# Optimization experiments

Hardware: AMD Instinct MI355X
Metric: run time of the kernel (lower is better)

Reference implementation:

```python
import jax, jax.numpy as jnp
import numpy as np

P = 64       # number of pathways
NV = 512     # features per pathway (nvar[i])
W = 256      # hidden width per pathway
COV = 16     # covariates
B = 2048     # batch
EPS = 1e-5   # BatchNorm eps
SLOPE = 0.2  # LeakyReLU negative slope


def _lrelu(v):
    return jnp.where(v >= 0, v, SLOPE * v)


def setup_inputs() -> dict:
    key = jax.random.key(0)
    ks = jax.random.split(key, 8)
    x = jax.random.normal(ks[0], (B, P * NV + COV), dtype=jnp.float32)
    # per-pathway weights (no bias), stacked across pathways -> grouped GEMM
    W1 = jax.random.normal(ks[1], (P, NV, W), dtype=jnp.float32) * (1.0 / np.sqrt(NV))
    W2 = jax.random.normal(ks[2], (P, W, W), dtype=jnp.float32) * (1.0 / np.sqrt(W))
    W3 = jax.random.normal(ks[3], (P, W), dtype=jnp.float32) * (1.0 / np.sqrt(W))
    gamma = jnp.ones((P,), dtype=jnp.float32)   # bn_path weight
    beta = jnp.zeros((P,), dtype=jnp.float32)   # bn_path bias
    fc_w = jax.random.normal(ks[4], (P + COV, 1), dtype=jnp.float32) * 0.05
    fc_b = jnp.full((1,), 0.001, dtype=jnp.float32)
    return {"x": x, "W1": W1, "W2": W2, "W3": W3,
            "gamma": gamma, "beta": beta, "fc_w": fc_w, "fc_b": fc_b}


def reference(x, W1, W2, W3, gamma, beta, fc_w, fc_b):
    # pathway blocks (dropout = identity in eval): grouped GEMMs over P pathways
    xp = x[:, : P * NV].reshape(B, P, NV)
    h = _lrelu(jnp.einsum('bpi,pio->bpo', xp, W1))
    h = _lrelu(jnp.einsum('bpi,pio->bpo', h, W2))
    p = _lrelu(jnp.einsum('bpi,pi->bp', h, W3))          # [B, P]
    # BatchNorm1d (training-mode batch statistics, biased variance)
    mean = p.mean(axis=0)
    var = p.var(axis=0)
    pn = (p - mean) / jnp.sqrt(var + EPS) * gamma + beta
    # global L2 (Frobenius) normalization, as torch.norm(pathway_layer, 2)
    pn = pn / jnp.linalg.norm(pn)
    # concat covariates, final linear + sigmoid
    z = jnp.concatenate([pn, x[:, P * NV: P * NV + COV]], axis=1)  # [B, P+COV]
    return jax.nn.sigmoid(z @ fc_w + fc_b)                         # [B, 1]
```

## Files before the change

### kernel.cpp

```cpp
#include <hip/hip_runtime.h>
#include <hip/hip_bf16.h>

#define PW 64
#define NV 512
#define HW 256
#define COV 16
#define BATCH 2048
#define XROW (PW * NV + COV)
#define IMG 16384

typedef short s16x8 __attribute__((ext_vector_type(8)));
typedef float f32x4 __attribute__((ext_vector_type(4)));

__device__ __forceinline__ unsigned short f2bf(float f) {
    union { float f; unsigned int u; } v;
    v.f = f;
    unsigned int u = v.u;
    unsigned int r = (u + 0x7fffu + ((u >> 16) & 1u)) >> 16;
    return (unsigned short)r;
}

__device__ __forceinline__ unsigned int pack2(float a, float b) {
    __hip_bfloat162 h = __float22bfloat162_rn(float2{a, b});
    union { __hip_bfloat162 h; unsigned int u; } c;
    c.h = h;
    return c.u;
}

__device__ __forceinline__ float lrelu(float v) { return v >= 0.f ? v : 0.2f * v; }

__device__ __forceinline__ void gl_lds16(const void* g, void* l) {
    __builtin_amdgcn_global_load_lds(
        (const __attribute__((address_space(1))) void*)g,
        (__attribute__((address_space(3))) void*)l, 16, 0, 0);
}

__global__ __launch_bounds__(256)
void transpose_all(const float* __restrict__ W1, const float* __restrict__ W2,
                   unsigned short* __restrict__ W1I, unsigned short* __restrict__ W2I) {
    __shared__ float tile[64][260];
    int bx = blockIdx.x;
    const float* src;
    unsigned short* dst;
    if (bx < 512) {
        int p = bx >> 3, kb = bx & 7;
        src = W1 + ((size_t)p * NV + kb * 64) * HW;
        dst = W1I + (size_t)(p * 8 + kb) * IMG;
    } else {
        bx -= 512;
        int p = bx >> 2, kb = bx & 3;
        src = W2 + ((size_t)p * HW + kb * 64) * HW;
        dst = W2I + (size_t)(p * 4 + kb) * IMG;
    }
    const int t = threadIdx.x;
    #pragma unroll
    for (int i = 0; i < 16; ++i) {
        int idx = t + i * 256;
        int r = idx >> 6, c4 = (idx & 63) << 2;
        *(float4*)&tile[r][c4] = *(const float4*)(src + (size_t)r * HW + c4);
    }
    __syncthreads();
    #pragma unroll
    for (int pass = 0; pass < 8; ++pass) {
        int idx = pass * 256 + t;
        int n = idx >> 3, s = idx & 7;
        int g = s ^ (n & 7);
        unsigned short v[8];
        #pragma unroll
        for (int j = 0; j < 8; ++j)
            v[j] = f2bf(tile[g * 8 + j][n]);
        *(s16x8*)(dst + (size_t)idx * 8) = *(s16x8*)v;
    }
}

__global__ __launch_bounds__(256, 2)
void pathway_fused(const float* __restrict__ x, const unsigned short* __restrict__ W1I,
                   const unsigned short* __restrict__ W2I, const float* __restrict__ W3,
                   float* __restrict__ pvec) {
    __shared__ __align__(16) unsigned short As[64][72];
    __shared__ __align__(16) unsigned short Bs[256 * 64];
    __shared__ __align__(16) unsigned short H1t[64][264];
    __shared__ float red[4][64];

    const int lin = blockIdx.x + blockIdx.y * (BATCH / 64);
    const int xcd = lin & 7;
    const int idx0 = lin >> 3;
    const int p   = xcd * 8 + (idx0 >> 5);
    const int bm0 = (idx0 & 31) * 64;

    const int t = threadIdx.x;
    const int lane = t & 63;
    const int wave = t >> 6;
    const int wn   = wave * 64;
    const int l15  = lane & 15;
    const int quad = lane >> 4;

    const float* Ap          = x   + (size_t)p * NV;
    const unsigned short* B1 = W1I + (size_t)p * 8 * IMG;
    const unsigned short* B2 = W2I + (size_t)p * 4 * IMG;

    {
        float4 aReg[4];
        #pragma unroll
        for (int i = 0; i < 4; ++i) {
            int ii = t + i * 256, row = ii >> 4, c4 = (ii & 15) * 4;
            aReg[i] = *(const float4*)(Ap + (size_t)(bm0 + row) * XROW + c4);
        }
        f32x4 acc[4][4] = {};
        for (int k0 = 0; k0 < NV; k0 += 64) {
            #pragma unroll
            for (int i = 0; i < 4; ++i) {
                int ii = t + i * 256, row = ii >> 4, c4 = (ii & 15) * 4;
                uint2 u;
                u.x = pack2(aReg[i].x, aReg[i].y);
                u.y = pack2(aReg[i].z, aReg[i].w);
                *(uint2*)&As[row][c4] = u;
            }
            {
                const unsigned short* img = B1 + (size_t)(k0 >> 6) * IMG;
                #pragma unroll
                for (int c = 0; c < 8; ++c) {
                    int off = wave * 8192 + c * 1024;
                    gl_lds16((const char*)img + off + lane * 16, (char*)Bs + off);
                }
            }
            __syncthreads();
            if (k0 + 64 < NV) {
                #pragma unroll
                for (int i = 0; i < 4; ++i) {
                    int ii = t + i * 256, row = ii >> 4, c4 = (ii & 15) * 4;
                    aReg[i] = *(const float4*)(Ap + (size_t)(bm0 + row) * XROW + k0 + 64 + c4);
                }
            }
            #pragma unroll
            for (int kk = 0; kk < 64; kk += 32) {
                s16x8 af[4], bfr[4];
                #pragma unroll
                for (int mi = 0; mi < 4; ++mi)
                    af[mi] = *(const s16x8*)&As[mi * 16 + l15][kk + quad * 8];
                #pragma unroll
                for (int ni = 0; ni < 4; ++ni) {
                    int row  = wn + ni * 16 + l15;
                    int slot = ((kk >> 3) + quad) ^ (row & 7);
                    bfr[ni] = *(const s16x8*)&Bs[row * 64 + slot * 8];
                }
                #pragma unroll
                for (int mi = 0; mi < 4; ++mi)
                    #pragma unroll
                    for (int ni = 0; ni < 4; ++ni)
                        acc[mi][ni] = __builtin_amdgcn_mfma_f32_16x16x32_bf16(
                            af[mi], bfr[ni], acc[mi][ni], 0, 0, 0);
            }
            __syncthreads();
        }
        #pragma unroll
        for (int mi = 0; mi < 4; ++mi)
            #pragma unroll
            for (int ni = 0; ni < 4; ++ni)
                #pragma unroll
                for (int r = 0; r < 4; ++r)
                    H1t[mi * 16 + quad * 4 + r][wn + ni * 16 + l15] =
                        f2bf(lrelu(acc[mi][ni][r]));
    }
    __syncthreads();

    f32x4 acc2[4][4] = {};
    for (int k0 = 0; k0 < HW; k0 += 64) {
        const unsigned short* img = B2 + (size_t)(k0 >> 6) * IMG;
        #pragma unroll
        for (int c = 0; c < 8; ++c) {
            int off = wave * 8192 + c * 1024;
            gl_lds16((const char*)img + off + lane * 16, (char*)Bs + off);
        }
        __syncthreads();
        #pragma unroll
        for (int kk = 0; kk < 64; kk += 32) {
            s16x8 af[4], bfr[4];
            #pragma unroll
            for (int mi = 0; mi < 4; ++mi)
                af[mi] = *(const s16x8*)&H1t[mi * 16 + l15][k0 + kk + quad * 8];
            #pragma unroll
            for (int ni = 0; ni < 4; ++ni) {
                int row  = wn + ni * 16 + l15;
                int slot = ((kk >> 3) + quad) ^ (row & 7);
                bfr[ni] = *(const s16x8*)&Bs[row * 64 + slot * 8];
            }
            #pragma unroll
            for (int mi = 0; mi < 4; ++mi)
                #pragma unroll
                for (int ni = 0; ni < 4; ++ni)
                    acc2[mi][ni] = __builtin_amdgcn_mfma_f32_16x16x32_bf16(
                        af[mi], bfr[ni], acc2[mi][ni], 0, 0, 0);
        }
        __syncthreads();
    }

    float w3v[4];
    #pragma unroll
    for (int ni = 0; ni < 4; ++ni)
        w3v[ni] = W3[(size_t)p * HW + wn + ni * 16 + l15];
    float part[4][4];
    #pragma unroll
    for (int mi = 0; mi < 4; ++mi) {
        #pragma unroll
        for (int r = 0; r < 4; ++r) {
            float s = 0.f;
            #pragma unroll
            for (int ni = 0; ni < 4; ++ni)
                s += lrelu(acc2[mi][ni][r]) * w3v[ni];
            part[mi][r] = s;
        }
    }
    #pragma unroll
    for (int off = 1; off < 16; off <<= 1)
        #pragma unroll
        for (int mi = 0; mi < 4; ++mi)
            #pragma unroll
            for (int r = 0; r < 4; ++r)
                part[mi][r] += __shfl_xor(part[mi][r], off);
    if (l15 == 0)
        #pragma unroll
        for (int mi = 0; mi < 4; ++mi)
            #pragma unroll
            for (int r = 0; r < 4; ++r)
                red[wave][mi * 16 + quad * 4 + r] = part[mi][r];
    __syncthreads();
    if (t < 64) {
        float s = red[0][t] + red[1][t] + red[2][t] + red[3][t];
        pvec[(size_t)p * BATCH + bm0 + t] = lrelu(s);
    }
}

__global__ __launch_bounds__(256)
void stats_k(const float* __restrict__ pvec, float* __restrict__ stat) {
    const int p = blockIdx.x;
    float s = 0.f, q = 0.f;
    for (int i = threadIdx.x; i < BATCH; i += 256) {
        float v = pvec[(size_t)p * BATCH + i];
        s += v; q += v * v;
    }
    #pragma unroll
    for (int off = 32; off; off >>= 1) {
        s += __shfl_down(s, off);
        q += __shfl_down(q, off);
    }
    __shared__ float ls[4], lq[4];
    const int wave = threadIdx.x >> 6, lane = threadIdx.x & 63;
    if (lane == 0) { ls[wave] = s; lq[wave] = q; }
    __syncthreads();
    if (threadIdx.x == 0) {
        float S = ls[0] + ls[1] + ls[2] + ls[3];
        float Q = lq[0] + lq[1] + lq[2] + lq[3];
        float mean = S * (1.f / BATCH);
        float var  = Q * (1.f / BATCH) - mean * mean;
        stat[p]       = mean;
        stat[64 + p]  = rsqrtf(var + 1e-5f);
        stat[128 + p] = var;
    }
}

__global__ __launch_bounds__(256)
void final_k(const float* __restrict__ pvec, const float* __restrict__ stat,
             const float* __restrict__ gamma, const float* __restrict__ beta,
             const float* __restrict__ x, const float* __restrict__ fc_w,
             const float* __restrict__ fc_b, float* __restrict__ out) {
    const int b = blockIdx.x * 256 + threadIdx.x;
    float nsq = 0.f;
    #pragma unroll
    for (int p = 0; p < PW; ++p) {
        float g = gamma[p], bt = beta[p], var = stat[128 + p], inv = stat[64 + p];
        nsq += (float)BATCH * (g * g * var * inv * inv + bt * bt);
    }
    const float rn = rsqrtf(nsq);
    float acc = fc_b[0];
    #pragma unroll
    for (int p = 0; p < PW; ++p) {
        float pn = (pvec[(size_t)p * BATCH + b] - stat[p]) * stat[64 + p] * gamma[p] + beta[p];
        acc += pn * rn * fc_w[p];
    }
    #pragma unroll
    for (int c = 0; c < COV; ++c)
        acc += x[(size_t)b * XROW + PW * NV + c] * fc_w[PW + c];
    out[b] = 1.f / (1.f + __expf(-acc));
}

extern "C" void kernel_launch(void* const* d_in, const int* in_sizes, int n_in,
                              void* d_out, int out_size, void* d_ws, size_t ws_size,
                              hipStream_t stream) {
    const float* x     = (const float*)d_in[0];
    const float* W1    = (const float*)d_in[1];
    const float* W2    = (const float*)d_in[2];
    const float* W3    = (const float*)d_in[3];
    const float* gamma = (const float*)d_in[4];
    const float* beta  = (const float*)d_in[5];
    const float* fc_w  = (const float*)d_in[6];
    const float* fc_b  = (const float*)d_in[7];
    float* out = (float*)d_out;

    char* ws = (char*)d_ws;
    size_t off = 0;
    unsigned short* W1I = (unsigned short*)(ws + off); off += (size_t)PW * NV * HW * 2;
    unsigned short* W2I = (unsigned short*)(ws + off); off += (size_t)PW * HW * HW * 2;
    float* pvec = (float*)(ws + off); off += (size_t)PW * BATCH * 4;
    float* stat = (float*)(ws + off); off += 256 * 4;

    transpose_all<<<dim3(512 + 256), 256, 0, stream>>>(W1, W2, W1I, W2I);

    pathway_fused<<<dim3(BATCH / 64, PW), 256, 0, stream>>>(x, W1I, W2I, W3, pvec);

    stats_k<<<PW, 256, 0, stream>>>(pvec, stat);

    final_k<<<BATCH / 256, 256, 0, stream>>>(pvec, stat, gamma, beta, x, fc_w, fc_b, out);
}
```

Baseline: 480.2 us.

## Split fused pathway kernel into double-buffered GEMM1 and GEMM2 kernels via bf16 intermediate

Splits the fused two-layer pathway kernel into two kernels. The first layer's bf16 activations now go to a global workspace in swizzled 64x64 tiles that the second kernel loads straight to LDS. Both kernels double-buffer their A and B tiles in shared memory, so the next k-slice's global loads overlap the current MFMA work instead of stalling on a single buffer. The cost is a 64 MB global round trip for the hidden activations and an extra kernel launch.

```diff
diff --git a/kernel.cpp b/kernel.cpp
--- a/kernel.cpp
+++ b/kernel.cpp
@@ -8,6 +8,7 @@
 #define BATCH 2048
 #define XROW (PW * NV + COV)
 #define IMG 16384
+#define AIMG 4096
 
 typedef short s16x8 __attribute__((ext_vector_type(8)));
 typedef float f32x4 __attribute__((ext_vector_type(4)));
@@ -74,19 +75,17 @@
 }
 
 __global__ __launch_bounds__(256, 2)
-void pathway_fused(const float* __restrict__ x, const unsigned short* __restrict__ W1I,
-                   const unsigned short* __restrict__ W2I, const float* __restrict__ W3,
-                   float* __restrict__ pvec) {
-    __shared__ __align__(16) unsigned short As[64][72];
-    __shared__ __align__(16) unsigned short Bs[256 * 64];
-    __shared__ __align__(16) unsigned short H1t[64][264];
-    __shared__ float red[4][64];
-
-    const int lin = blockIdx.x + blockIdx.y * (BATCH / 64);
+void gemm1(const float* __restrict__ x, const unsigned short* __restrict__ W1I,
+           unsigned short* __restrict__ H1I) {
+    __shared__ __align__(16) unsigned short As[2][64 * 64];
+    __shared__ __align__(16) unsigned short Bs[2][256 * 64];
+
+    const int lin = blockIdx.x;
     const int xcd = lin & 7;
-    const int idx0 = lin >> 3;
-    const int p   = xcd * 8 + (idx0 >> 5);
-    const int bm0 = (idx0 & 31) * 64;
+    const int idx = lin >> 3;
+    const int p   = xcd * 8 + (idx >> 5);
+    const int m   = idx & 31;
+    const int bm0 = m * 64;
 
     const int t = threadIdx.x;
     const int lane = t & 63;
@@ -97,104 +96,176 @@
 
     const float* Ap          = x   + (size_t)p * NV;
     const unsigned short* B1 = W1I + (size_t)p * 8 * IMG;
-    const unsigned short* B2 = W2I + (size_t)p * 4 * IMG;
-
-    {
-        float4 aReg[4];
-        #pragma unroll
-        for (int i = 0; i < 4; ++i) {
-            int ii = t + i * 256, row = ii >> 4, c4 = (ii & 15) * 4;
-            aReg[i] = *(const float4*)(Ap + (size_t)(bm0 + row) * XROW + c4);
-        }
-        f32x4 acc[4][4] = {};
-        for (int k0 = 0; k0 < NV; k0 += 64) {
+
+    int arow[4], acol[4], aoff[4];
+    #pragma unroll
+    for (int i = 0; i < 4; ++i) {
+        int ii = t + i * 256;
+        arow[i] = ii >> 4;
+        acol[i] = (ii & 15) * 4;
+        int slot = (acol[i] >> 3) ^ (arow[i] & 7);
+        aoff[i] = arow[i] * 64 + slot * 8 + (acol[i] & 7);
+    }
+
+    float4 aA[4], aB[4];
+
+#define XLOAD(dst, k0) { \
+    _Pragma("unroll") \
+    for (int i = 0; i < 4; ++i) \
+        dst[i] = *(const float4*)(Ap + (size_t)(bm0 + arow[i]) * XROW + (k0) + acol[i]); }
+
+#define APACK(src, buf) { \
+    _Pragma("unroll") \
+    for (int i = 0; i < 4; ++i) { \
+        uint2 u; \
+        u.x = pack2(src[i].x, src[i].y); \
+        u.y = pack2(src[i].z, src[i].w); \
+        *(uint2*)&As[buf][aoff[i]] = u; } }
+
+#define B1STAGE(buf, kb) { \
+    const unsigned short* img = B1 + (size_t)(kb) * IMG; \
+    _Pragma("unroll") \
+    for (int c = 0; c < 8; ++c) { \
+        int off = wave * 8192 + c * 1024; \
+        gl_lds16((const char*)img + off + lane * 16, (char*)Bs[buf] + off); } }
+
+#define MFMA1(buf) { \
+    _Pragma("unroll") \
+    for (int kk = 0; kk < 64; kk += 32) { \
+        s16x8 af[4], bfr[4]; \
+        _Pragma("unroll") \
+        for (int mi = 0; mi < 4; ++mi) { \
+            int row = mi * 16 + l15; \
+            int slot = ((kk >> 3) + quad) ^ (row & 7); \
+            af[mi] = *(const s16x8*)&As[buf][row * 64 + slot * 8]; } \
+        _Pragma("unroll") \
+        for (int ni = 0; ni < 4; ++ni) { \
+            int row = wn + ni * 16 + l15; \
+            int slot = ((kk >> 3) + quad) ^ (row & 7); \
+            bfr[ni] = *(const s16x8*)&Bs[buf][row * 64 + slot * 8]; } \
+        _Pragma("unroll") \
+        for (int mi = 0; mi < 4; ++mi) \
+            _Pragma("unroll") \
+            for (int ni = 0; ni < 4; ++ni) \
+                acc[mi][ni] = __builtin_amdgcn_mfma_f32_16x16x32_bf16( \
+                    af[mi], bfr[ni], acc[mi][ni], 0, 0, 0); } }
+
+    XLOAD(aA, 0);
+    B1STAGE(0, 0);
+    APACK(aA, 0);
+    XLOAD(aA, 64);
+    __syncthreads();
+
+    f32x4 acc[4][4] = {};
+
+    #pragma unroll
+    for (int s2 = 0; s2 < 4; ++s2) {
+        const int te = 2 * s2;
+        if (te + 1 < 8) B1STAGE((te + 1) & 1, te + 1);
+        if (te + 2 < 8) XLOAD(aB, (te + 2) * 64);
+        MFMA1(te & 1);
+        if (te + 1 < 8) APACK(aA, (te + 1) & 1);
+        __syncthreads();
+        const int to = te + 1;
+        if (to + 1 < 8) B1STAGE((to + 1) & 1, to + 1);
+        if (to + 2 < 8) XLOAD(aA, (to + 2) * 64);
+        MFMA1(to & 1);
+        if (to + 1 < 8) APACK(aB, (to + 1) & 1);
+        __syncthreads();
+    }
+
+    unsigned short* Hp = H1I + ((size_t)(p * 32 + m) * 4 + wave) * AIMG;
+    #pragma unroll
+    for (int mi = 0; mi < 4; ++mi)
+        #pragma unroll
+        for (int ni = 0; ni < 4; ++ni)
             #pragma unroll
-            for (int i = 0; i < 4; ++i) {
-                int ii = t + i * 256, row = ii >> 4, c4 = (ii & 15) * 4;
-                uint2 u;
-                u.x = pack2(aReg[i].x, aReg[i].y);
-                u.y = pack2(aReg[i].z, aReg[i].w);
-                *(uint2*)&As[row][c4] = u;
+            for (int r = 0; r < 4; ++r) {
+                int row = mi * 16 + quad * 4 + r;
+                int col = ni * 16 + l15;
+                int slot = (col >> 3) ^ (row & 7);
+                Hp[row * 64 + slot * 8 + (col & 7)] = f2bf(lrelu(acc[mi][ni][r]));
             }
-            {
-                const unsigned short* img = B1 + (size_t)(k0 >> 6) * IMG;
-                #pragma unroll
-                for (int c = 0; c < 8; ++c) {
-                    int off = wave * 8192 + c * 1024;
-                    gl_lds16((const char*)img + off + lane * 16, (char*)Bs + off);
-                }
-            }
-            __syncthreads();
-            if (k0 + 64 < NV) {
-                #pragma unroll
-                for (int i = 0; i < 4; ++i) {
-                    int ii = t + i * 256, row = ii >> 4, c4 = (ii & 15) * 4;
-                    aReg[i] = *(const float4*)(Ap + (size_t)(bm0 + row) * XROW + k0 + 64 + c4);
-                }
-            }
-            #pragma unroll
-            for (int kk = 0; kk < 64; kk += 32) {
-                s16x8 af[4], bfr[4];
-                #pragma unroll
-                for (int mi = 0; mi < 4; ++mi)
-                    af[mi] = *(const s16x8*)&As[mi * 16 + l15][kk + quad * 8];
-                #pragma unroll
-                for (int ni = 0; ni < 4; ++ni) {
-                    int row  = wn + ni * 16 + l15;
-                    int slot = ((kk >> 3) + quad) ^ (row & 7);
-                    bfr[ni] = *(const s16x8*)&Bs[row * 64 + slot * 8];
-                }
-                #pragma unroll
-                for (int mi = 0; mi < 4; ++mi)
-                    #pragma unroll
-                    for (int ni = 0; ni < 4; ++ni)
-                        acc[mi][ni] = __builtin_amdgcn_mfma_f32_16x16x32_bf16(
-                            af[mi], bfr[ni], acc[mi][ni], 0, 0, 0);
-            }
-            __syncthreads();
-        }
-        #pragma unroll
-        for (int mi = 0; mi < 4; ++mi)
-            #pragma unroll
-            for (int ni = 0; ni < 4; ++ni)
-                #pragma unroll
-                for (int r = 0; r < 4; ++r)
-                    H1t[mi * 16 + quad * 4 + r][wn + ni * 16 + l15] =
-                        f2bf(lrelu(acc[mi][ni][r]));
-    }
-    __syncthreads();
-
-    f32x4 acc2[4][4] = {};
-    for (int k0 = 0; k0 < HW; k0 += 64) {
-        const unsigned short* img = B2 + (size_t)(k0 >> 6) * IMG;
-        #pragma unroll
-        for (int c = 0; c < 8; ++c) {
-            int off = wave * 8192 + c * 1024;
-            gl_lds16((const char*)img + off + lane * 16, (char*)Bs + off);
-        }
+#undef XLOAD
+#undef APACK
+#undef B1STAGE
+#undef MFMA1
+}
+
+__global__ __launch_bounds__(256, 2)
+void gemm2(const unsigned short* __restrict__ H1I, const unsigned short* __restrict__ W2I,
+           const float* __restrict__ W3, float* __restrict__ pvec) {
+    __shared__ __align__(16) unsigned short As[2][64 * 64];
+    __shared__ __align__(16) unsigned short Bs[2][256 * 64];
+
+    const int lin = blockIdx.x;
+    const int xcd = lin & 7;
+    const int idx = lin >> 3;
+    const int p   = xcd * 8 + (idx >> 5);
+    const int m   = idx & 31;
+    const int bm0 = m * 64;
+
+    const int t = threadIdx.x;
+    const int lane = t & 63;
+    const int wave = t >> 6;
+    const int wn   = wave * 64;
+    const int l15  = lane & 15;
+    const int quad = lane >> 4;
+
+    const unsigned short* Aimg = H1I + (size_t)(p * 32 + m) * 4 * AIMG;
+    const unsigned short* B2   = W2I + (size_t)p * 4 * IMG;
+
+#define A2STAGE(buf, kb) { \
+    const unsigned short* img = Aimg + (size_t)(kb) * AIMG; \
+    _Pragma("unroll") \
+    for (int c = 0; c < 2; ++c) { \
+        int off = wave * 2048 + c * 1024; \
+        gl_lds16((const char*)img + off + lane * 16, (char*)As[buf] + off); } }
+
+#define B2STAGE(buf, kb) { \
+    const unsigned short* img = B2 + (size_t)(kb) * IMG; \
+    _Pragma("unroll") \
+    for (int c = 0; c < 8; ++c) { \
+        int off = wave * 8192 + c * 1024; \
+        gl_lds16((const char*)img + off + lane * 16, (char*)Bs[buf] + off); } }
+
+#define MFMA2(buf) { \
+    _Pragma("unroll") \
+    for (int kk = 0; kk < 64; kk += 32) { \
+        s16x8 af[4], bfr[4]; \
+        _Pragma("unroll") \
+        for (int mi = 0; mi < 4; ++mi) { \
+            int row = mi * 16 + l15; \
+            int slot = ((kk >> 3) + quad) ^ (row & 7); \
+            af[mi] = *(const s16x8*)&As[buf][row * 64 + slot * 8]; } \
+        _Pragma("unroll") \
+        for (int ni = 0; ni < 4; ++ni) { \
+            int row = wn + ni * 16 + l15; \
+            int slot = ((kk >> 3) + quad) ^ (row & 7); \
+            bfr[ni] = *(const s16x8*)&Bs[buf][row * 64 + slot * 8]; } \
+        _Pragma("unroll") \
+        for (int mi = 0; mi < 4; ++mi) \
+            _Pragma("unroll") \
+            for (int ni = 0; ni < 4; ++ni) \
+                acc[mi][ni] = __builtin_amdgcn_mfma_f32_16x16x32_bf16( \
+                    af[mi], bfr[ni], acc[mi][ni], 0, 0, 0); } }
+
+    A2STAGE(0, 0);
+    B2STAGE(0, 0);
+    __syncthreads();
+
+    f32x4 acc[4][4] = {};
+    #pragma unroll
+    for (int t4 = 0; t4 < 4; ++t4) {
+        if (t4 + 1 < 4) { A2STAGE((t4 + 1) & 1, t4 + 1); B2STAGE((t4 + 1) & 1, t4 + 1); }
+        MFMA2(t4 & 1);
         __syncthreads();
-        #pragma unroll
-        for (int kk = 0; kk < 64; kk += 32) {
-            s16x8 af[4], bfr[4];
-            #pragma unroll
-            for (int mi = 0; mi < 4; ++mi)
-                af[mi] = *(const s16x8*)&H1t[mi * 16 + l15][k0 + kk + quad * 8];
-            #pragma unroll
-            for (int ni = 0; ni < 4; ++ni) {
-                int row  = wn + ni * 16 + l15;
-                int slot = ((kk >> 3) + quad) ^ (row & 7);
-                bfr[ni] = *(const s16x8*)&Bs[row * 64 + slot * 8];
-            }
-            #pragma unroll
-            for (int mi = 0; mi < 4; ++mi)
-                #pragma unroll
-                for (int ni = 0; ni < 4; ++ni)
-                    acc2[mi][ni] = __builtin_amdgcn_mfma_f32_16x16x32_bf16(
-                        af[mi], bfr[ni], acc2[mi][ni], 0, 0, 0);
-        }
-        __syncthreads();
-    }
-
+    }
+#undef A2STAGE
+#undef B2STAGE
+#undef MFMA2
+
+    float* red = (float*)&As[0][0];
     float w3v[4];
     #pragma unroll
     for (int ni = 0; ni < 4; ++ni)
@@ -207,7 +278,7 @@
             float s = 0.f;
             #pragma unroll
             for (int ni = 0; ni < 4; ++ni)
-                s += lrelu(acc2[mi][ni][r]) * w3v[ni];
+                s += lrelu(acc[mi][ni][r]) * w3v[ni];
             part[mi][r] = s;
         }
     }
@@ -223,10 +294,10 @@
         for (int mi = 0; mi < 4; ++mi)
             #pragma unroll
             for (int r = 0; r < 4; ++r)
-                red[wave][mi * 16 + quad * 4 + r] = part[mi][r];
+                red[wave * 64 + mi * 16 + quad * 4 + r] = part[mi][r];
     __syncthreads();
     if (t < 64) {
-        float s = red[0][t] + red[1][t] + red[2][t] + red[3][t];
+        float s = red[0 * 64 + t] + red[1 * 64 + t] + red[2 * 64 + t] + red[3 * 64 + t];
         pvec[(size_t)p * BATCH + bm0 + t] = lrelu(s);
     }
 }
@@ -301,12 +372,15 @@
     size_t off = 0;
     unsigned short* W1I = (unsigned short*)(ws + off); off += (size_t)PW * NV * HW * 2;
     unsigned short* W2I = (unsigned short*)(ws + off); off += (size_t)PW * HW * HW * 2;
+    unsigned short* H1I = (unsigned short*)(ws + off); off += (size_t)PW * BATCH * HW * 2;
     float* pvec = (float*)(ws + off); off += (size_t)PW * BATCH * 4;
     float* stat = (float*)(ws + off); off += 256 * 4;
 
     transpose_all<<<dim3(512 + 256), 256, 0, stream>>>(W1, W2, W1I, W2I);
 
-    pathway_fused<<<dim3(BATCH / 64, PW), 256, 0, stream>>>(x, W1I, W2I, W3, pvec);
+    gemm1<<<dim3(2048), 256, 0, stream>>>(x, W1I, H1I);
+
+    gemm2<<<dim3(2048), 256, 0, stream>>>(H1I, W2I, W3, pvec);
 
     stats_k<<<PW, 256, 0, stream>>>(pvec, stat);
 
```

New measurement: 509.4 us. +6.1%, slower.
